# Kernel optimization log

Hardware: AMD Instinct MI355X
Metric: run time of the kernel (lower is better)

The kernel has to match this reference:

```python
import jax, jax.numpy as jnp
import numpy as np

B, S1, S2, D, H, FFN = 4, 1024, 1024, 1024, 16, 4096
DK = D // H  # 64
EPS = 1e-5


def layer_norm(x, g, b):
    m = jnp.mean(x, axis=-1, keepdims=True)
    v = jnp.mean((x - m) ** 2, axis=-1, keepdims=True)
    return (x - m) * jax.lax.rsqrt(v + EPS) * g + b


def cross_attention(y, kvn, mask, qw, kw, vw, ow, ob):
    # y: [B,S1,D], kvn: [B,S2,D], mask: [B,S2] int (0 -> masked)
    q = (y @ qw).reshape(B, S1, H, DK)
    k = (kvn @ kw).reshape(B, S2, H, DK)
    v = (kvn @ vw).reshape(B, S2, H, DK)
    attn = jnp.einsum('bqhd,bkhd->bhqk', q, k) / np.sqrt(DK).astype(np.float32)
    attn = jnp.where(mask[:, None, None, :] == 0, jnp.float32(-1e9), attn)
    attn = jax.nn.softmax(attn, axis=-1)
    out = jnp.einsum('bhqk,bkhd->bqhd', attn, v).reshape(B, S1, H * DK)
    return out @ ow + ob


def setup_inputs() -> dict:
    key = jax.random.key(0)
    ks = jax.random.split(key, 16)
    s = 1.0 / np.sqrt(D)
    inp = {
        'x': jax.random.normal(ks[0], (B, S1, D), jnp.float32),
        'kv': jax.random.normal(ks[1], (B, S2, D), jnp.float32),
        'attn_bias': jax.random.randint(ks[2], (B, S2), 0, 2, jnp.int32),
        'ln1_g': jnp.ones((D,), jnp.float32),
        'ln1_b': jnp.zeros((D,), jnp.float32),
        'qw0': jax.random.normal(ks[3], (D, D), jnp.float32) * s,
        'kw0': jax.random.normal(ks[4], (D, D), jnp.float32) * s,
        'vw0': jax.random.normal(ks[5], (D, D), jnp.float32) * s,
        'ow0': jax.random.normal(ks[6], (D, D), jnp.float32) * s,
        'ob0': jnp.zeros((D,), jnp.float32),
        'qw1': jax.random.normal(ks[7], (D, D), jnp.float32) * s,
        'kw1': jax.random.normal(ks[8], (D, D), jnp.float32) * s,
        'vw1': jax.random.normal(ks[9], (D, D), jnp.float32) * s,
        'ow1': jax.random.normal(ks[10], (D, D), jnp.float32) * s,
        'ob1': jnp.zeros((D,), jnp.float32),
        'ln2_g': jnp.ones((D,), jnp.float32),
        'ln2_b': jnp.zeros((D,), jnp.float32),
        'w1': jax.random.normal(ks[11], (D, FFN), jnp.float32) * s,
        'b1': jnp.zeros((FFN,), jnp.float32),
        'w2': jax.random.normal(ks[12], (FFN, D), jnp.float32) * (1.0 / np.sqrt(FFN)),
        'b2': jnp.zeros((D,), jnp.float32),
    }
    return inp


def reference(x, kv, attn_bias, ln1_g, ln1_b, qw0, kw0, vw0, ow0, ob0,
              qw1, kw1, vw1, ow1, ob1, ln2_g, ln2_b, w1, b1, w2, b2):
    y = layer_norm(x, ln1_g, ln1_b)
    kvn = layer_norm(kv, ln1_g, ln1_b)  # same norm module applied to both
    y = cross_attention(y, kvn, attn_bias, qw0, kw0, vw0, ow0, ob0) + y
    y = cross_attention(y, kvn, attn_bias, qw1, kw1, vw1, ow1, ob1) + y
    x = x + y  # dropout rate 0 -> identity
    y = layer_norm(x, ln2_g, ln2_b)
    y = jax.nn.relu(y @ w1 + b1) @ w2 + b2
    x = x + y
    return x
```

## Files before the change

kernel.cpp:

```cpp
#include <hip/hip_runtime.h>
#include <stdint.h>

typedef unsigned short u16;
typedef __bf16 bf16x8 __attribute__((ext_vector_type(8)));
typedef float f32x4 __attribute__((ext_vector_type(4)));

#define LOG2E 1.4426950408889634f

__device__ __forceinline__ float bf2f(u16 a) {
  union { unsigned u; float f; } v; v.u = ((unsigned)a) << 16; return v.f;
}
__device__ __forceinline__ u16 f2bf(float f) {
  union { float f; unsigned u; } v; v.f = f;
  unsigned r = v.u + 0x7fffu + ((v.u >> 16) & 1u);
  return (u16)(r >> 16);
}
__device__ __forceinline__ u16 f2bf_fast(float f) {
  __bf16 h = (__bf16)f;
  union { __bf16 h; u16 u; } v; v.h = h; return v.u;
}
__device__ __forceinline__ void gl_lds16(const void* g, void* l) {
  __builtin_amdgcn_global_load_lds(
      (const __attribute__((address_space(1))) uint32_t*)g,
      (__attribute__((address_space(3))) uint32_t*)l,
      16, 0, 0);
}

__device__ __forceinline__ int swz(int row, int colu16) {
  return row * 64 + (colu16 ^ (((row ^ (row >> 2)) & 7) << 3));
}

template <int BM, int BN, int MODE>
__global__ __launch_bounds__(256) void gemm_bt(
    const u16* __restrict__ A, const u16* __restrict__ Bt,
    u16* Cbf, float* C32,
    const float* __restrict__ bias,
    const u16* resbf, const float* __restrict__ resx,
    int M, int N, int K)
{
  constexpr int MT = BM / 32, NT = BN / 32;
  constexpr int GA = BM / 32, GB = BN / 32;
  __shared__ u16 sA[BM * 64];
  __shared__ u16 sB[BN * 64];
  const int tid  = threadIdx.x;
  const int wave = tid >> 6, lane = tid & 63;
  const int quad = lane >> 4, l16 = lane & 15;
  const int wm = wave >> 1, wn = wave & 1;
  const int m0 = blockIdx.y * BM, n0 = blockIdx.x * BN;

  f32x4 acc[MT][NT] = {};

  for (int k0 = 0; k0 < K; k0 += 64) {
    __syncthreads();
#pragma unroll
    for (int i = 0; i < GA; ++i) {
      int cb = i * 256 + wave * 64;
      int c = cb + lane;
      int row = c >> 3, kc = c & 7;
      gl_lds16(A + (size_t)(m0 + row) * K + k0 + kc * 8, &sA[cb * 8]);
    }
#pragma unroll
    for (int i = 0; i < GB; ++i) {
      int cb = i * 256 + wave * 64;
      int c = cb + lane;
      int row = c >> 3, kc = c & 7;
      gl_lds16(Bt + (size_t)(n0 + row) * K + k0 + kc * 8, &sB[cb * 8]);
    }
    __syncthreads();

#pragma unroll
    for (int kk = 0; kk < 2; ++kk) {
      bf16x8 fa[MT], fb[NT];
#pragma unroll
      for (int mt = 0; mt < MT; ++mt)
        fa[mt] = *(const bf16x8*)&sA[(wm * (BM / 2) + mt * 16 + l16) * 64 + kk * 32 + quad * 8];
#pragma unroll
      for (int nt = 0; nt < NT; ++nt)
        fb[nt] = *(const bf16x8*)&sB[(wn * (BN / 2) + nt * 16 + l16) * 64 + kk * 32 + quad * 8];
#pragma unroll
      for (int mt = 0; mt < MT; ++mt)
#pragma unroll
        for (int nt = 0; nt < NT; ++nt)
          acc[mt][nt] = __builtin_amdgcn_mfma_f32_16x16x32_bf16(
              fa[mt], fb[nt], acc[mt][nt], 0, 0, 0);
    }
  }

#pragma unroll
  for (int mt = 0; mt < MT; ++mt) {
#pragma unroll
    for (int nt = 0; nt < NT; ++nt) {
#pragma unroll
      for (int r = 0; r < 4; ++r) {
        int row = m0 + wm * (BM / 2) + mt * 16 + quad * 4 + r;
        int col = n0 + wn * (BN / 2) + nt * 16 + l16;
        size_t idx = (size_t)row * N + col;
        float v = acc[mt][nt][r];
        if constexpr (MODE == 0) {
          Cbf[idx] = f2bf(v);
        } else if constexpr (MODE == 1) {
          v += bias[col] + bf2f(resbf[idx]);
          Cbf[idx] = f2bf(v);
        } else if constexpr (MODE == 2) {
          v = fmaxf(v + bias[col], 0.f);
          Cbf[idx] = f2bf(v);
        } else if constexpr (MODE == 3) {
          v += bias[col] + resx[idx] + bf2f(resbf[idx]);
          C32[idx] = v;
        } else {
          C32[idx] = C32[idx] + v;
        }
      }
    }
  }
}

__global__ __launch_bounds__(256) void transpose64(
    const float* __restrict__ in, u16* __restrict__ out, int R, int Cstride)
{
  __shared__ u16 tile[64][72];
  const int r0 = blockIdx.y * 64, c0 = blockIdx.x * 64;
  const int t = threadIdx.x;
  {
    const int lr = t >> 4, lc = (t & 15) * 4;
#pragma unroll
    for (int h = 0; h < 4; ++h) {
      int row = h * 16 + lr;
      float4 vd = *(const float4*)&in[(size_t)(r0 + row) * Cstride + c0 + lc];
      ushort4 ov;
      ov.x = f2bf(vd.x); ov.y = f2bf(vd.y); ov.z = f2bf(vd.z); ov.w = f2bf(vd.w);
      *(ushort4*)&tile[row][lc] = ov;
    }
  }
  __syncthreads();
  {
    const int lr = t >> 3, lv = t & 7;
#pragma unroll
    for (int h = 0; h < 2; ++h) {
      int orow = h * 32 + lr;
      u16 tmp[8];
#pragma unroll
      for (int j = 0; j < 8; ++j) tmp[j] = tile[lv * 8 + j][orow];
      *(uint4*)&out[(size_t)(c0 + orow) * R + r0 + lv * 8] = *(uint4*)tmp;
    }
  }
}

__global__ __launch_bounds__(256) void vt_kernel(
    const u16* __restrict__ in, u16* __restrict__ out)
{
  __shared__ u16 tile[64][72];
  const int st = blockIdx.x, bh = blockIdx.y;
  const int b = bh >> 4, h = bh & 15;
  const int t = threadIdx.x;
  const int lr = t >> 3, lv = t & 7;
  const u16* src = in + ((size_t)b * 1024 + st * 64) * 2048 + 1024 + h * 64;
#pragma unroll
  for (int half = 0; half < 2; ++half) {
    int row = half * 32 + lr;
    uint4 vd = *(const uint4*)&src[(size_t)row * 2048 + lv * 8];
    *(uint4*)&tile[row][lv * 8] = vd;
  }
  __syncthreads();
  u16* dst = out + (size_t)bh * 64 * 1024 + st * 64;
#pragma unroll
  for (int half = 0; half < 2; ++half) {
    int orow = half * 32 + lr;
    u16 tmp[8];
#pragma unroll
    for (int j = 0; j < 8; ++j) tmp[j] = tile[lv * 8 + j][orow];
    *(uint4*)&dst[(size_t)orow * 1024 + lv * 8] = *(uint4*)tmp;
  }
}

__global__ __launch_bounds__(256) void ln_kernel(
    const float* __restrict__ x, const float* __restrict__ g,
    const float* __restrict__ b, u16* __restrict__ outbf)
{
  const int row = blockIdx.x, t = threadIdx.x;
  const int wave = t >> 6, lane = t & 63;
  float4 xv = *(const float4*)&x[(size_t)row * 1024 + t * 4];
  float v0 = xv.x, v1 = xv.y, v2 = xv.z, v3 = xv.w;
  float s = v0 + v1 + v2 + v3;
  float s2 = v0 * v0 + v1 * v1 + v2 * v2 + v3 * v3;
  for (int m = 1; m < 64; m <<= 1) { s += __shfl_xor(s, m); s2 += __shfl_xor(s2, m); }
  __shared__ float ps[4], pq[4];
  if (lane == 0) { ps[wave] = s; pq[wave] = s2; }
  __syncthreads();
  s = ps[0] + ps[1] + ps[2] + ps[3];
  s2 = pq[0] + pq[1] + pq[2] + pq[3];
  float mean = s * (1.f / 1024.f);
  float var = s2 * (1.f / 1024.f) - mean * mean;
  float rs = rsqrtf(var + 1e-5f);
  float4 gv = *(const float4*)&g[t * 4];
  float4 bv = *(const float4*)&b[t * 4];
  ushort4 ov;
  ov.x = f2bf((v0 - mean) * rs * gv.x + bv.x);
  ov.y = f2bf((v1 - mean) * rs * gv.y + bv.y);
  ov.z = f2bf((v2 - mean) * rs * gv.z + bv.z);
  ov.w = f2bf((v3 - mean) * rs * gv.w + bv.w);
  *(ushort4*)&outbf[(size_t)row * 1024 + t * 4] = ov;
}

__global__ __launch_bounds__(256) void ln_add_kernel(
    const float* __restrict__ x, const u16* __restrict__ ybf,
    const float* __restrict__ g, const float* __restrict__ b,
    u16* __restrict__ hbf)
{
  const int row = blockIdx.x, t = threadIdx.x;
  const int wave = t >> 6, lane = t & 63;
  float4 xv = *(const float4*)&x[(size_t)row * 1024 + t * 4];
  ushort4 yv = *(const ushort4*)&ybf[(size_t)row * 1024 + t * 4];
  float v0 = xv.x + bf2f(yv.x), v1 = xv.y + bf2f(yv.y);
  float v2 = xv.z + bf2f(yv.z), v3 = xv.w + bf2f(yv.w);
  float s = v0 + v1 + v2 + v3;
  float s2 = v0 * v0 + v1 * v1 + v2 * v2 + v3 * v3;
  for (int m = 1; m < 64; m <<= 1) { s += __shfl_xor(s, m); s2 += __shfl_xor(s2, m); }
  __shared__ float ps[4], pq[4];
  if (lane == 0) { ps[wave] = s; pq[wave] = s2; }
  __syncthreads();
  s = ps[0] + ps[1] + ps[2] + ps[3];
  s2 = pq[0] + pq[1] + pq[2] + pq[3];
  float mean = s * (1.f / 1024.f);
  float var = s2 * (1.f / 1024.f) - mean * mean;
  float rs = rsqrtf(var + 1e-5f);
  float4 gv = *(const float4*)&g[t * 4];
  float4 bv = *(const float4*)&b[t * 4];
  ushort4 ov;
  ov.x = f2bf((v0 - mean) * rs * gv.x + bv.x);
  ov.y = f2bf((v1 - mean) * rs * gv.y + bv.y);
  ov.z = f2bf((v2 - mean) * rs * gv.z + bv.z);
  ov.w = f2bf((v3 - mean) * rs * gv.w + bv.w);
  *(ushort4*)&hbf[(size_t)row * 1024 + t * 4] = ov;
}

__global__ __launch_bounds__(256) void attn_kernel(
    const u16* __restrict__ Q,
    const u16* __restrict__ K,
    const u16* __restrict__ Vt,
    const int* __restrict__ mask,
    u16* __restrict__ O)
{
  __shared__ u16 sK[64 * 64], sVt[64 * 64], sP[64 * 64];
  __shared__ float smaskf[64];
  const int qt = blockIdx.x, h = blockIdx.y, b = blockIdx.z;
  const int t = threadIdx.x;
  const int wave = t >> 6, lane = t & 63;
  const int quad = lane >> 4, l16 = lane & 15;
  const u16* Qb = Q + (size_t)b * 1024 * 1024 + (size_t)qt * 64 * 1024 + h * 64;
  const u16* Kb = K + (size_t)b * 1024 * 2048 + h * 64;
  const u16* Vb = Vt + (size_t)(b * 16 + h) * 64 * 1024;

#pragma unroll
  for (int i = 0; i < 2; ++i) {
    int cb = i * 256 + wave * 64;
    int c = cb + lane;
    int row = c >> 3;
    int scc = (c & 7) ^ ((row ^ (row >> 2)) & 7);
    gl_lds16(Qb + (size_t)row * 1024 + scc * 8, &sP[cb * 8]);
  }
  __syncthreads();
  bf16x8 aq[2];
#pragma unroll
  for (int ks = 0; ks < 2; ++ks)
    aq[ks] = *(const bf16x8*)&sP[swz(wave * 16 + l16, ks * 32 + quad * 8)];

  float m2_[4], l_[4];
  f32x4 accO[4] = {};
#pragma unroll
  for (int r = 0; r < 4; ++r) { m2_[r] = -1e30f; l_[r] = 0.f; }

  constexpr float QS = 0.125f * LOG2E;

  for (int j = 0; j < 16; ++j) {
    __syncthreads();
#pragma unroll
    for (int i = 0; i < 2; ++i) {
      int cb = i * 256 + wave * 64;
      int c = cb + lane;
      int row = c >> 3;
      int scc = (c & 7) ^ ((row ^ (row >> 2)) & 7);
      gl_lds16(Kb + (size_t)(j * 64 + row) * 2048 + scc * 8, &sK[cb * 8]);
      gl_lds16(Vb + (size_t)row * 1024 + j * 64 + scc * 8, &sVt[cb * 8]);
    }
    if (t < 64) smaskf[t] = (mask[b * 1024 + j * 64 + t] == 0) ? -1e9f : 0.f;
    __syncthreads();

    f32x4 accS[4] = {};
#pragma unroll
    for (int ks = 0; ks < 2; ++ks) {
#pragma unroll
      for (int nt = 0; nt < 4; ++nt) {
        bf16x8 bk = *(const bf16x8*)&sK[swz(nt * 16 + l16, ks * 32 + quad * 8)];
        accS[nt] = __builtin_amdgcn_mfma_f32_16x16x32_bf16(aq[ks], bk, accS[nt], 0, 0, 0);
      }
    }
    float mf[4];
#pragma unroll
    for (int nt = 0; nt < 4; ++nt) mf[nt] = smaskf[nt * 16 + l16];

    float vv[4][4], cm_[4];
    bool need = false;
#pragma unroll
    for (int r = 0; r < 4; ++r) {
#pragma unroll
      for (int nt = 0; nt < 4; ++nt) vv[r][nt] = fmaf(accS[nt][r], QS, mf[nt]);
      float cm = fmaxf(fmaxf(vv[r][0], vv[r][1]), fmaxf(vv[r][2], vv[r][3]));
      for (int sh = 1; sh < 16; sh <<= 1) cm = fmaxf(cm, __shfl_xor(cm, sh));
      cm_[r] = cm;
      need = need || (cm > m2_[r] + 8.f);
    }
    if (__any(need)) {
#pragma unroll
      for (int r = 0; r < 4; ++r) {
        float nm = fmaxf(m2_[r], cm_[r]);
        float al = exp2f(m2_[r] - nm);
        m2_[r] = nm;
        l_[r] *= al;
#pragma unroll
        for (int n2 = 0; n2 < 4; ++n2) accO[n2][r] *= al;
      }
    }
#pragma unroll
    for (int r = 0; r < 4; ++r) {
      int prow = wave * 16 + quad * 4 + r;
      float rs = 0.f;
#pragma unroll
      for (int nt = 0; nt < 4; ++nt) {
        float p = exp2f(vv[r][nt] - m2_[r]);
        rs += p;
        sP[swz(prow, nt * 16 + l16)] = f2bf_fast(p);
      }
      l_[r] += rs;
    }
    __syncthreads();
#pragma unroll
    for (int ks = 0; ks < 2; ++ks) {
      bf16x8 ap = *(const bf16x8*)&sP[swz(wave * 16 + l16, ks * 32 + quad * 8)];
#pragma unroll
      for (int n2 = 0; n2 < 4; ++n2) {
        bf16x8 bvv = *(const bf16x8*)&sVt[swz(n2 * 16 + l16, ks * 32 + quad * 8)];
        accO[n2] = __builtin_amdgcn_mfma_f32_16x16x32_bf16(ap, bvv, accO[n2], 0, 0, 0);
      }
    }
  }

  u16* Ob = O + (size_t)b * 1024 * 1024 + (size_t)qt * 64 * 1024 + h * 64;
#pragma unroll
  for (int r = 0; r < 4; ++r) {
    float lr = l_[r];
    for (int sh = 1; sh < 16; sh <<= 1) lr += __shfl_xor(lr, sh);
    float inv = 1.f / lr;
    int row = wave * 16 + quad * 4 + r;
#pragma unroll
    for (int n2 = 0; n2 < 4; ++n2)
      Ob[(size_t)row * 1024 + n2 * 16 + l16] = f2bf_fast(accO[n2][r] * inv);
  }
}

extern "C" void kernel_launch(void* const* d_in, const int* in_sizes, int n_in,
                              void* d_out, int out_size, void* d_ws, size_t ws_size,
                              hipStream_t stream)
{
  const float* x   = (const float*)d_in[0];
  const float* kv  = (const float*)d_in[1];
  const int* attn_bias = (const int*)d_in[2];
  const float* ln1_g = (const float*)d_in[3];
  const float* ln1_b = (const float*)d_in[4];
  const float* qw0 = (const float*)d_in[5];
  const float* kw0 = (const float*)d_in[6];
  const float* vw0 = (const float*)d_in[7];
  const float* ow0 = (const float*)d_in[8];
  const float* ob0 = (const float*)d_in[9];
  const float* qw1 = (const float*)d_in[10];
  const float* kw1 = (const float*)d_in[11];
  const float* vw1 = (const float*)d_in[12];
  const float* ow1 = (const float*)d_in[13];
  const float* ob1 = (const float*)d_in[14];
  const float* ln2_g = (const float*)d_in[15];
  const float* ln2_b = (const float*)d_in[16];
  const float* w1 = (const float*)d_in[17];
  const float* b1 = (const float*)d_in[18];
  const float* w2 = (const float*)d_in[19];
  const float* b2 = (const float*)d_in[20];

  char* ws = (char*)d_ws;
  const size_t MB = 1u << 20;
  u16* Wkv   = (u16*)(ws + 0 * MB);
  u16* Wsm   = (u16*)(ws + 4 * MB);
  u16* wtA   = (u16*)(ws + 0 * MB);
  u16* wtB   = (u16*)(ws + 4 * MB);
  u16* ybf   = (u16*)(ws + 8 * MB);
  u16* kvnbf = (u16*)(ws + 16 * MB);
  u16* qbuf  = (u16*)(ws + 24 * MB);
  u16* kvbuf = (u16*)(ws + 32 * MB);
  u16* hbf   = kvnbf;
  u16* fbuf  = kvbuf;
  u16* attnb = (u16*)d_out;
  u16* vT    = (u16*)((char*)d_out + 8 * MB);
  float* out32 = (float*)d_out;

  const dim3 B256(256);
  const dim3 gT(16, 16);
  const dim3 gGemmN1k(8, 64);
  const dim3 gGemm2k(16, 32);
  const dim3 gVt(16, 64);
  const dim3 gAttn(16, 16, 4);

  ln_kernel<<<4096, B256, 0, stream>>>(x,  ln1_g, ln1_b, ybf);
  ln_kernel<<<4096, B256, 0, stream>>>(kv, ln1_g, ln1_b, kvnbf);

  for (int layer = 0; layer < 2; ++layer) {
    const float* qw = layer ? qw1 : qw0;
    const float* kw = layer ? kw1 : kw0;
    const float* vw = layer ? vw1 : vw0;
    const float* ow = layer ? ow1 : ow0;
    const float* ob = layer ? ob1 : ob0;

    transpose64<<<gT, B256, 0, stream>>>(kw, Wkv, 1024, 1024);
    transpose64<<<gT, B256, 0, stream>>>(vw, Wkv + 1024 * 1024, 1024, 1024);
    gemm_bt<128, 128, 0><<<gGemm2k, B256, 0, stream>>>(
        kvnbf, Wkv, kvbuf, nullptr, nullptr, nullptr, nullptr, 4096, 2048, 1024);
    transpose64<<<gT, B256, 0, stream>>>(qw, Wsm, 1024, 1024);
    gemm_bt<64, 128, 0><<<gGemmN1k, B256, 0, stream>>>(
        ybf, Wsm, qbuf, nullptr, nullptr, nullptr, nullptr, 4096, 1024, 1024);
    vt_kernel<<<gVt, B256, 0, stream>>>(kvbuf, vT);

    attn_kernel<<<gAttn, B256, 0, stream>>>(qbuf, kvbuf, vT, attn_bias, attnb);

    transpose64<<<gT, B256, 0, stream>>>(ow, Wsm, 1024, 1024);
    gemm_bt<64, 128, 1><<<gGemmN1k, B256, 0, stream>>>(
        attnb, Wsm, ybf, nullptr, ob, ybf, nullptr, 4096, 1024, 1024);
  }

  ln_add_kernel<<<4096, B256, 0, stream>>>(x, ybf, ln2_g, ln2_b, hbf);

  for (int band = 0; band < 2; ++band) {
    transpose64<<<dim3(32, 16), B256, 0, stream>>>(w1 + band * 2048, wtA, 1024, 4096);
    transpose64<<<dim3(16, 32), B256, 0, stream>>>(w2 + (size_t)band * 2048 * 1024,
                                                   wtB, 2048, 1024);
    gemm_bt<128, 128, 2><<<gGemm2k, B256, 0, stream>>>(
        hbf, wtA, fbuf, nullptr, b1 + band * 2048, nullptr, nullptr,
        4096, 2048, 1024);
    if (band == 0) {
      gemm_bt<64, 128, 3><<<gGemmN1k, B256, 0, stream>>>(
          fbuf, wtB, nullptr, out32, b2, ybf, x, 4096, 1024, 2048);
    } else {
      gemm_bt<64, 128, 4><<<gGemmN1k, B256, 0, stream>>>(
          fbuf, wtB, nullptr, out32, nullptr, nullptr, nullptr, 4096, 1024, 2048);
    }
  }
}
```

Baseline: 632.9 us.

## Process 128 query rows per attention block to halve K/V tile reloads

The attention kernel now has each block handle 128 query rows instead of 64, with each wave owning two 16-row groups. Each K/V tile loaded into LDS therefore feeds twice as much MFMA work, and the P·V step reuses the loaded V fragments across both groups. The grid is reordered so head is the fastest-varying block index, and the barrier between writing and reading P is dropped because each wave only touches its own rows. The cost is more registers per thread and half as many blocks in the grid, which lowers occupancy and the parallelism available to hide latency.

```diff
diff --git a/kernel.cpp b/kernel.cpp
--- a/kernel.cpp
+++ b/kernel.cpp
@@ -241,18 +241,18 @@
     const int* __restrict__ mask,
     u16* __restrict__ O)
 {
-  __shared__ u16 sK[64 * 64], sVt[64 * 64], sP[64 * 64];
+  __shared__ u16 sK[64 * 64], sVt[64 * 64], sP[128 * 64];
   __shared__ float smaskf[64];
-  const int qt = blockIdx.x, h = blockIdx.y, b = blockIdx.z;
+  const int h = blockIdx.x, qt = blockIdx.y, b = blockIdx.z;
   const int t = threadIdx.x;
   const int wave = t >> 6, lane = t & 63;
   const int quad = lane >> 4, l16 = lane & 15;
-  const u16* Qb = Q + (size_t)b * 1024 * 1024 + (size_t)qt * 64 * 1024 + h * 64;
+  const u16* Qb = Q + (size_t)b * 1024 * 1024 + (size_t)qt * 128 * 1024 + h * 64;
   const u16* Kb = K + (size_t)b * 1024 * 2048 + h * 64;
   const u16* Vb = Vt + (size_t)(b * 16 + h) * 64 * 1024;
 
 #pragma unroll
-  for (int i = 0; i < 2; ++i) {
+  for (int i = 0; i < 4; ++i) {
     int cb = i * 256 + wave * 64;
     int c = cb + lane;
     int row = c >> 3;
@@ -260,15 +260,19 @@
     gl_lds16(Qb + (size_t)row * 1024 + scc * 8, &sP[cb * 8]);
   }
   __syncthreads();
-  bf16x8 aq[2];
-#pragma unroll
-  for (int ks = 0; ks < 2; ++ks)
-    aq[ks] = *(const bf16x8*)&sP[swz(wave * 16 + l16, ks * 32 + quad * 8)];
-
-  float m2_[4], l_[4];
-  f32x4 accO[4] = {};
-#pragma unroll
-  for (int r = 0; r < 4; ++r) { m2_[r] = -1e30f; l_[r] = 0.f; }
+  bf16x8 aq[2][2];
+#pragma unroll
+  for (int g = 0; g < 2; ++g)
+#pragma unroll
+    for (int ks = 0; ks < 2; ++ks)
+      aq[g][ks] = *(const bf16x8*)&sP[swz(wave * 32 + g * 16 + l16, ks * 32 + quad * 8)];
+
+  float m2_[2][4], l_[2][4];
+  f32x4 accO[2][4] = {};
+#pragma unroll
+  for (int g = 0; g < 2; ++g)
+#pragma unroll
+    for (int r = 0; r < 4; ++r) { m2_[g][r] = -1e30f; l_[g][r] = 0.f; }
 
   constexpr float QS = 0.125f * LOG2E;
 
@@ -286,75 +290,85 @@
     if (t < 64) smaskf[t] = (mask[b * 1024 + j * 64 + t] == 0) ? -1e9f : 0.f;
     __syncthreads();
 
-    f32x4 accS[4] = {};
+    float mf[4];
+#pragma unroll
+    for (int nt = 0; nt < 4; ++nt) mf[nt] = smaskf[nt * 16 + l16];
+
+#pragma unroll
+    for (int g = 0; g < 2; ++g) {
+      f32x4 accS[4] = {};
+#pragma unroll
+      for (int ks = 0; ks < 2; ++ks) {
+#pragma unroll
+        for (int nt = 0; nt < 4; ++nt) {
+          bf16x8 bk = *(const bf16x8*)&sK[swz(nt * 16 + l16, ks * 32 + quad * 8)];
+          accS[nt] = __builtin_amdgcn_mfma_f32_16x16x32_bf16(aq[g][ks], bk, accS[nt], 0, 0, 0);
+        }
+      }
+      float vv[4][4], cm_[4];
+      bool need = false;
+#pragma unroll
+      for (int r = 0; r < 4; ++r) {
+#pragma unroll
+        for (int nt = 0; nt < 4; ++nt) vv[r][nt] = fmaf(accS[nt][r], QS, mf[nt]);
+        float cm = fmaxf(fmaxf(vv[r][0], vv[r][1]), fmaxf(vv[r][2], vv[r][3]));
+        for (int sh = 1; sh < 16; sh <<= 1) cm = fmaxf(cm, __shfl_xor(cm, sh));
+        cm_[r] = cm;
+        need = need || (cm > m2_[g][r] + 8.f);
+      }
+      if (__any(need)) {
+#pragma unroll
+        for (int r = 0; r < 4; ++r) {
+          float nm = fmaxf(m2_[g][r], cm_[r]);
+          float al = exp2f(m2_[g][r] - nm);
+          m2_[g][r] = nm;
+          l_[g][r] *= al;
+#pragma unroll
+          for (int n2 = 0; n2 < 4; ++n2) accO[g][n2][r] *= al;
+        }
+      }
+#pragma unroll
+      for (int r = 0; r < 4; ++r) {
+        int prow = wave * 32 + g * 16 + quad * 4 + r;
+        float rs = 0.f;
+#pragma unroll
+        for (int nt = 0; nt < 4; ++nt) {
+          float p = exp2f(vv[r][nt] - m2_[g][r]);
+          rs += p;
+          sP[swz(prow, nt * 16 + l16)] = f2bf_fast(p);
+        }
+        l_[g][r] += rs;
+      }
+    }
 #pragma unroll
     for (int ks = 0; ks < 2; ++ks) {
-#pragma unroll
-      for (int nt = 0; nt < 4; ++nt) {
-        bf16x8 bk = *(const bf16x8*)&sK[swz(nt * 16 + l16, ks * 32 + quad * 8)];
-        accS[nt] = __builtin_amdgcn_mfma_f32_16x16x32_bf16(aq[ks], bk, accS[nt], 0, 0, 0);
-      }
-    }
-    float mf[4];
-#pragma unroll
-    for (int nt = 0; nt < 4; ++nt) mf[nt] = smaskf[nt * 16 + l16];
-
-    float vv[4][4], cm_[4];
-    bool need = false;
+      bf16x8 bv[4];
+#pragma unroll
+      for (int n2 = 0; n2 < 4; ++n2)
+        bv[n2] = *(const bf16x8*)&sVt[swz(n2 * 16 + l16, ks * 32 + quad * 8)];
+#pragma unroll
+      for (int g = 0; g < 2; ++g) {
+        bf16x8 ap = *(const bf16x8*)&sP[swz(wave * 32 + g * 16 + l16, ks * 32 + quad * 8)];
+#pragma unroll
+        for (int n2 = 0; n2 < 4; ++n2)
+          accO[g][n2] = __builtin_amdgcn_mfma_f32_16x16x32_bf16(ap, bv[n2], accO[g][n2], 0, 0, 0);
+      }
+    }
+  }
+
+  u16* Ob = O + (size_t)b * 1024 * 1024 + (size_t)qt * 128 * 1024 + h * 64;
+#pragma unroll
+  for (int g = 0; g < 2; ++g) {
 #pragma unroll
     for (int r = 0; r < 4; ++r) {
-#pragma unroll
-      for (int nt = 0; nt < 4; ++nt) vv[r][nt] = fmaf(accS[nt][r], QS, mf[nt]);
-      float cm = fmaxf(fmaxf(vv[r][0], vv[r][1]), fmaxf(vv[r][2], vv[r][3]));
-      for (int sh = 1; sh < 16; sh <<= 1) cm = fmaxf(cm, __shfl_xor(cm, sh));
-      cm_[r] = cm;
-      need = need || (cm > m2_[r] + 8.f);
-    }
-    if (__any(need)) {
-#pragma unroll
-      for (int r = 0; r < 4; ++r) {
-        float nm = fmaxf(m2_[r], cm_[r]);
-        float al = exp2f(m2_[r] - nm);
-        m2_[r] = nm;
-        l_[r] *= al;
-#pragma unroll
-        for (int n2 = 0; n2 < 4; ++n2) accO[n2][r] *= al;
-      }
-    }
-#pragma unroll
-    for (int r = 0; r < 4; ++r) {
-      int prow = wave * 16 + quad * 4 + r;
-      float rs = 0.f;
-#pragma unroll
-      for (int nt = 0; nt < 4; ++nt) {
-        float p = exp2f(vv[r][nt] - m2_[r]);
-        rs += p;
-        sP[swz(prow, nt * 16 + l16)] = f2bf_fast(p);
-      }
-      l_[r] += rs;
-    }
-    __syncthreads();
-#pragma unroll
-    for (int ks = 0; ks < 2; ++ks) {
-      bf16x8 ap = *(const bf16x8*)&sP[swz(wave * 16 + l16, ks * 32 + quad * 8)];
-#pragma unroll
-      for (int n2 = 0; n2 < 4; ++n2) {
-        bf16x8 bvv = *(const bf16x8*)&sVt[swz(n2 * 16 + l16, ks * 32 + quad * 8)];
-        accO[n2] = __builtin_amdgcn_mfma_f32_16x16x32_bf16(ap, bvv, accO[n2], 0, 0, 0);
-      }
-    }
-  }
-
-  u16* Ob = O + (size_t)b * 1024 * 1024 + (size_t)qt * 64 * 1024 + h * 64;
-#pragma unroll
-  for (int r = 0; r < 4; ++r) {
-    float lr = l_[r];
-    for (int sh = 1; sh < 16; sh <<= 1) lr += __shfl_xor(lr, sh);
-    float inv = 1.f / lr;
-    int row = wave * 16 + quad * 4 + r;
-#pragma unroll
-    for (int n2 = 0; n2 < 4; ++n2)
-      Ob[(size_t)row * 1024 + n2 * 16 + l16] = f2bf_fast(accO[n2][r] * inv);
+      float lr = l_[g][r];
+      for (int sh = 1; sh < 16; sh <<= 1) lr += __shfl_xor(lr, sh);
+      float inv = 1.f / lr;
+      int row = wave * 32 + g * 16 + quad * 4 + r;
+#pragma unroll
+      for (int n2 = 0; n2 < 4; ++n2)
+        Ob[(size_t)row * 1024 + n2 * 16 + l16] = f2bf_fast(accO[g][n2][r] * inv);
+    }
   }
 }
 
@@ -405,7 +419,7 @@
   const dim3 gGemmN1k(8, 64);
   const dim3 gGemm2k(16, 32);
   const dim3 gVt(16, 64);
-  const dim3 gAttn(16, 16, 4);
+  const dim3 gAttn(16, 8, 4);
 
   ln_kernel<<<4096, B256, 0, stream>>>(x,  ln1_g, ln1_b, ybf);
   ln_kernel<<<4096, B256, 0, stream>>>(kv, ln1_g, ln1_b, kvnbf);
```

New measurement: 616.7 us. -2.6%, faster.
